# Kernel optimization log

Measured on AMD Instinct MI355X. Metric: run time of the kernel, lower is better.

Reference implementation:

```python
import jax, jax.numpy as jnp
import numpy as np

N_NODES = 1000000
N_EDGES = 2000000
N_FEAT = 11          # QM9 num_features
HIDDEN = 64
N_CLASSES = 19       # QM9 num_classes
BATCH = 128


def setup_inputs() -> dict:
    key = jax.random.key(0)
    k = jax.random.split(key, 8)
    x = jax.random.normal(k[0], (N_NODES, N_FEAT), dtype=jnp.float32)
    edge_index = jax.random.randint(k[1], (2, N_EDGES), 0, N_NODES, dtype=jnp.int64)
    y = jax.random.normal(k[2], (BATCH, N_CLASSES), dtype=jnp.float32)
    batch = jnp.sort(jax.random.randint(k[3], (N_NODES,), 0, BATCH, dtype=jnp.int64))
    # GCNConv params: weight [in, hidden], bias [hidden]
    W_conv = jax.random.normal(k[4], (N_FEAT, HIDDEN), dtype=jnp.float32) / np.sqrt(N_FEAT)
    b_conv = jnp.zeros((HIDDEN,), dtype=jnp.float32)
    # Final linear: [hidden, classes]
    W_lin = jax.random.normal(k[5], (HIDDEN, N_CLASSES), dtype=jnp.float32) / np.sqrt(HIDDEN)
    b_lin = jnp.zeros((N_CLASSES,), dtype=jnp.float32)
    return {"x": x, "edge_index": edge_index, "y": y, "batch": batch,
            "W_conv": W_conv, "b_conv": b_conv, "W_lin": W_lin, "b_lin": b_lin}


def reference(x, edge_index, y, batch, W_conv, b_conv, W_lin, b_lin):
    row, col = edge_index[0], edge_index[1]  # source -> target
    # GCN symmetric normalization (add_self_loops=False): deg over targets
    ones = jnp.ones((edge_index.shape[1],), dtype=x.dtype)
    deg = jax.ops.segment_sum(ones, col, num_segments=N_NODES)
    dinv = jnp.where(deg > 0, jax.lax.rsqrt(jnp.maximum(deg, 1.0)), 0.0)
    norm = dinv[row] * dinv[col]  # [E]
    # Transform then aggregate: gather at source, scatter-add at target
    xw = x @ W_conv                                    # [N, H]
    msgs = xw[row] * norm[:, None]                     # [E, H]
    agg = jax.ops.segment_sum(msgs, col, num_segments=N_NODES) + b_conv
    h = jax.nn.relu(agg)                               # [N, H]
    # global_mean_pool over batch ids (size=BATCH)
    summed = jax.ops.segment_sum(h, batch, num_segments=BATCH)   # [B, H]
    counts = jax.ops.segment_sum(jnp.ones((N_NODES,), dtype=x.dtype), batch, num_segments=BATCH)
    pooled = summed / jnp.maximum(counts, 1.0)[:, None]
    # dropout p=0.5 is identity in eval mode
    return pooled @ W_lin + b_lin                      # [B, classes]
```

## Files before the change

kernel.cpp:

```cpp
#include <hip/hip_runtime.h>

#define N_NODES   1000000
#define N_EDGES   2000000
#define N_FEAT    11
#define HIDDEN    64
#define BATCH     128
#define N_CLASSES 19

#define NPB     2048
#define NBUCK   489
#define BCAP    5120
#define EPB     8192
#define PBLK    245
#define NSLOT   8
#define NCHUNK  3907
#define FROW    24
#define ZOFF    (256 * FROW)

typedef __attribute__((ext_vector_type(8))) short v8s;
typedef __attribute__((ext_vector_type(4))) float v4f;

__device__ __forceinline__ unsigned f2b(float v) {
    unsigned u = __float_as_uint(v);
    return (u + 0x7FFFu + ((u >> 16) & 1u)) >> 16;
}

__global__ __launch_bounds__(1024) void part_kernel(const int* __restrict__ row,
                                                    const int* __restrict__ col,
                                                    int* __restrict__ bcnt,
                                                    int* __restrict__ part) {
    __shared__ int lh[512];
    const int t = threadIdx.x;
    if (t < 512) lh[t] = 0;
    __syncthreads();
    const int q0 = (blockIdx.x * EPB) >> 2;
    const int4* col4 = (const int4*)col;
    const int4* row4 = (const int4*)row;
    const int qa = q0 + t, qb = q0 + 1024 + t;
    const bool va = qa < N_EDGES / 4, vb = qb < N_EDGES / 4;
    int4 ca, ra, cb, rb;
    if (va) { ca = col4[qa]; ra = row4[qa]; }
    if (vb) { cb = col4[qb]; rb = row4[qb]; }
    if (va) {
        atomicAdd(&lh[ca.x >> 11], 1); atomicAdd(&lh[ca.y >> 11], 1);
        atomicAdd(&lh[ca.z >> 11], 1); atomicAdd(&lh[ca.w >> 11], 1);
    }
    if (vb) {
        atomicAdd(&lh[cb.x >> 11], 1); atomicAdd(&lh[cb.y >> 11], 1);
        atomicAdd(&lh[cb.z >> 11], 1); atomicAdd(&lh[cb.w >> 11], 1);
    }
    __syncthreads();
    if (t < NBUCK) {
        int v = lh[t];
        if (v) lh[t] = t * BCAP + atomicAdd(&bcnt[t], v);
    }
    __syncthreads();
    int p;
    if (va) {
        p = atomicAdd(&lh[ca.x >> 11], 1); part[p] = (ra.x << 11) | (ca.x & (NPB - 1));
        p = atomicAdd(&lh[ca.y >> 11], 1); part[p] = (ra.y << 11) | (ca.y & (NPB - 1));
        p = atomicAdd(&lh[ca.z >> 11], 1); part[p] = (ra.z << 11) | (ca.z & (NPB - 1));
        p = atomicAdd(&lh[ca.w >> 11], 1); part[p] = (ra.w << 11) | (ca.w & (NPB - 1));
    }
    if (vb) {
        p = atomicAdd(&lh[cb.x >> 11], 1); part[p] = (rb.x << 11) | (cb.x & (NPB - 1));
        p = atomicAdd(&lh[cb.y >> 11], 1); part[p] = (rb.y << 11) | (cb.y & (NPB - 1));
        p = atomicAdd(&lh[cb.z >> 11], 1); part[p] = (rb.z << 11) | (cb.z & (NPB - 1));
        p = atomicAdd(&lh[cb.w >> 11], 1); part[p] = (rb.w << 11) | (cb.w & (NPB - 1));
    }
}

__global__ __launch_bounds__(512) void sort2_kernel(const int* __restrict__ part,
                                                    const int* __restrict__ bcnt,
                                                    const float* __restrict__ x,
                                                    int* __restrict__ srcs,
                                                    int* __restrict__ nstart,
                                                    unsigned short* __restrict__ ndeg,
                                                    float* __restrict__ dinv,
                                                    unsigned short* __restrict__ xs) {
    __shared__ int cnt[NPB];
    __shared__ int off[NPB];
    __shared__ int tsum[512];
    __shared__ int stage[BCAP];
    const int t = threadIdx.x, b = blockIdx.x;
    for (int i = t; i < NPB; i += 512) cnt[i] = 0;
    __syncthreads();
    const int s0 = b * BCAP, e0 = s0 + bcnt[b];
    for (int j = s0 + t; j < e0; j += 512)
        atomicAdd(&cnt[part[j] & (NPB - 1)], 1);
    __syncthreads();
    const int i0 = t * 4;
    int c[4], s = 0;
#pragma unroll
    for (int q = 0; q < 4; ++q) { c[q] = cnt[i0 + q]; s += c[q]; }
    tsum[t] = s;
    __syncthreads();
    for (int o = 1; o < 512; o <<= 1) {
        int a = (t >= o) ? tsum[t - o] : 0;
        __syncthreads();
        tsum[t] += a;
        __syncthreads();
    }
    int run = tsum[t] - s;
#pragma unroll
    for (int q = 0; q < 4; ++q) { off[i0 + q] = run; run += c[q]; }
    __syncthreads();
    for (int i = t; i < NPB; i += 512) {
        int n = b * NPB + i;
        if (n < N_NODES) {
            int d = cnt[i];
            float dv = d ? rsqrtf((float)d) : 0.0f;
            dinv[n]   = dv;
            ndeg[n]   = (unsigned short)d;
            nstart[n] = s0 + off[i];
            const float* xr = x + (size_t)n * N_FEAT;
            unsigned h[11];
#pragma unroll
            for (int k = 0; k < 11; ++k) h[k] = f2b(dv * xr[k]);
            uint4 A, B;
            A.x = h[0] | (h[1] << 16); A.y = h[2] | (h[3] << 16);
            A.z = h[4] | (h[5] << 16); A.w = h[6] | (h[7] << 16);
            B.x = h[8] | (h[9] << 16); B.y = h[10]; B.z = 0u; B.w = 0u;
            uint4* o = (uint4*)(xs + (size_t)n * 16);
            o[0] = A; o[1] = B;
        }
    }
    __syncthreads();
    for (int j = s0 + t; j < e0; j += 512) {
        int p  = part[j];
        int cl = p & (NPB - 1);
        int pos = atomicAdd(&off[cl], 1);
        stage[pos] = p >> 11;
    }
    __syncthreads();
    const int m = e0 - s0;
    const int m4 = m >> 2;
    int4* d4 = (int4*)(srcs + s0);
    const int4* s4 = (const int4*)stage;
    for (int j = t; j < m4; j += 512) d4[j] = s4[j];
    for (int j = (m4 << 2) + t; j < m; j += 512) srcs[s0 + j] = stage[j];
}

__global__ __launch_bounds__(256) void gather_pool_kernel(
    const int* __restrict__ srcs, const unsigned short* __restrict__ xs,
    const int* __restrict__ nstart, const unsigned short* __restrict__ ndeg,
    const float* __restrict__ dinv, const int* __restrict__ batch,
    const float* __restrict__ Wc, const float* __restrict__ bc,
    float* __restrict__ pooled, float* __restrict__ countsf) {
    __shared__ unsigned short fb16[ZOFF + 8];
    __shared__ int   sj0[256];
    __shared__ int   sdeg[256];
    __shared__ float sdinv[256];
    __shared__ int   sbid[256];
    __shared__ int   sperm[256];
    __shared__ int   dcnt[32];
    __shared__ int   doff[32];
    __shared__ float pbuf[2 * HIDDEN];
    __shared__ int   pcnt[NSLOT];
    const int t = threadIdx.x, lane = t & 63, w = t >> 6;
    const int quad = lane >> 4;
    const int base = blockIdx.x * 256;
    {
        int n = base + t;
        bool v = n < N_NODES;
        sj0[t]   = v ? nstart[n] : 0;
        sdeg[t]  = v ? (int)ndeg[n] : 0;
        sdinv[t] = v ? dinv[n] : 0.0f;
        sbid[t]  = v ? batch[n] : -1;
    }
    if (t < 2 * HIDDEN) pbuf[t] = 0.0f;
    if (t < NSLOT) pcnt[t] = 0;
    if (t < 32)    dcnt[t] = 0;
    if (t < 4)     ((unsigned*)(fb16 + ZOFF))[t] = 0u;
    __syncthreads();
    const int bid0 = sbid[0];
    {
        int bid = sbid[t];
        if (bid >= 0) {
            int slot = bid - bid0;
            if (slot >= 0 && slot < NSLOT) atomicAdd(&pcnt[slot], 1);
            else atomicAdd(&countsf[bid], 1.0f);
        }
    }
    int mybin = sdeg[t] < 31 ? sdeg[t] : 31;
    atomicAdd(&dcnt[mybin], 1);
    __syncthreads();
    if (t < 32) {
        int r = 0;
        for (int i = 0; i < t; ++i) r += dcnt[i];
        doff[t] = r;
    }
    __syncthreads();
    int pos = atomicAdd(&doff[mybin], 1);
    sperm[pos] = t;
    __syncthreads();

    {
        int i  = sperm[t];
        int j0 = sj0[i], d = sdeg[i];
        float acc[11];
#pragma unroll
        for (int k = 0; k < 11; ++k) acc[k] = 0.0f;
        for (int j = j0; j < j0 + d; ++j) {
            int r = srcs[j];
            const uint4* xr = (const uint4*)(xs + (size_t)r * 16);
            uint4 A = xr[0];
            uint2 B = *(const uint2*)(xr + 1);
            acc[0]  += __uint_as_float(A.x << 16);
            acc[1]  += __uint_as_float(A.x & 0xFFFF0000u);
            acc[2]  += __uint_as_float(A.y << 16);
            acc[3]  += __uint_as_float(A.y & 0xFFFF0000u);
            acc[4]  += __uint_as_float(A.z << 16);
            acc[5]  += __uint_as_float(A.z & 0xFFFF0000u);
            acc[6]  += __uint_as_float(A.w << 16);
            acc[7]  += __uint_as_float(A.w & 0xFFFF0000u);
            acc[8]  += __uint_as_float(B.x << 16);
            acc[9]  += __uint_as_float(B.x & 0xFFFF0000u);
            acc[10] += __uint_as_float(B.y << 16);
        }
        unsigned hb[11];
#pragma unroll
        for (int k = 0; k < 11; ++k) hb[k] = f2b(acc[k]);
        uint4 U0, U1;
        U0.x = hb[0] | (hb[1] << 16); U0.y = hb[2]  | (hb[3] << 16);
        U0.z = hb[4] | (hb[5] << 16); U0.w = hb[6]  | (hb[7] << 16);
        U1.x = hb[8] | (hb[9] << 16); U1.y = hb[10]; U1.z = 0u; U1.w = 0u;
        uint4* wp = (uint4*)(fb16 + i * FROW);
        wp[0] = U0; wp[1] = U1;
    }
    __syncthreads();

    const int nch = w * 16 + (lane & 15);
    union { v8s v; unsigned short us[8]; } bf;
#pragma unroll
    for (int j = 0; j < 8; ++j) {
        int k = quad * 8 + j;
        bf.us[j] = (k < 11) ? (unsigned short)f2b(Wc[k * HIDDEN + nch]) : (unsigned short)0;
    }
    const float bias_lane = bc[nch];
    float acc0 = 0.0f, acc1 = 0.0f;
#pragma unroll 4
    for (int mtile = 0; mtile < 16; ++mtile) {
        const v8s* ap = (quad < 2)
            ? (const v8s*)(fb16 + (mtile * 16 + (lane & 15)) * FROW + quad * 8)
            : (const v8s*)(fb16 + ZOFF);
        v8s a = *ap;
        v4f d = __builtin_amdgcn_mfma_f32_16x16x32_bf16(a, bf.v, (v4f){0.f, 0.f, 0.f, 0.f}, 0, 0, 0);
#pragma unroll
        for (int r = 0; r < 4; ++r) {
            int node = mtile * 16 + quad * 4 + r;
            int bid  = sbid[node];
            if (bid >= 0) {
                float h = fmaxf(fmaf(sdinv[node], d[r], bias_lane), 0.0f);
                int slot = bid - bid0;
                if (slot == 0)      acc0 += h;
                else if (slot == 1) acc1 += h;
                else atomicAdd(&pooled[(size_t)bid * HIDDEN + nch], h);
            }
        }
    }
    atomicAdd(&pbuf[nch], acc0);
    atomicAdd(&pbuf[HIDDEN + nch], acc1);
    __syncthreads();
    for (int s = w; s < 2; s += 4) {
        int c = pcnt[s];
        if (c > 0) {
            atomicAdd(&pooled[(size_t)(bid0 + s) * HIDDEN + lane], pbuf[s * HIDDEN + lane]);
            if (lane == 0) atomicAdd(&countsf[bid0 + s], (float)c);
        }
    }
}

__global__ void final_kernel(const float* __restrict__ pooled, const float* __restrict__ counts,
                             const float* __restrict__ Wl, const float* __restrict__ bl,
                             float* __restrict__ out) {
    int i = blockIdx.x * blockDim.x + threadIdx.x;
    if (i >= BATCH * N_CLASSES) return;
    int b = i / N_CLASSES;
    int c = i - b * N_CLASSES;
    float inv = 1.0f / fmaxf(counts[b], 1.0f);
    float s = bl[c];
#pragma unroll 8
    for (int h = 0; h < HIDDEN; ++h)
        s = fmaf(pooled[b * HIDDEN + h] * inv, Wl[h * N_CLASSES + c], s);
    out[i] = s;
}

extern "C" void kernel_launch(void* const* d_in, const int* in_sizes, int n_in,
                              void* d_out, int out_size, void* d_ws, size_t ws_size,
                              hipStream_t stream) {
    const float* x     = (const float*)d_in[0];
    const int*   ei    = (const int*)d_in[1];
    const int*   batch = (const int*)d_in[3];
    const float* Wc    = (const float*)d_in[4];
    const float* bc    = (const float*)d_in[5];
    const float* Wl    = (const float*)d_in[6];
    const float* bl    = (const float*)d_in[7];
    float*       out   = (float*)d_out;

    int*            bcnt    = (int*)d_ws;
    float*          pooled  = (float*)(bcnt + 512);
    float*          countsf = pooled + BATCH * HIDDEN;
    unsigned short* xs      = (unsigned short*)(countsf + BATCH);
    int*            nstart  = (int*)(xs + (size_t)N_NODES * 16);
    unsigned short* ndeg    = (unsigned short*)(nstart + N_NODES);
    float*          dinv    = (float*)(ndeg + N_NODES);
    int*            part    = (int*)(dinv + N_NODES);
    int*            srcs    = part + (size_t)NBUCK * BCAP;

    size_t zero_bytes = (512 + BATCH * HIDDEN + BATCH) * 4;
    hipMemsetAsync(d_ws, 0, zero_bytes, stream);

    const int* row = ei;
    const int* col = ei + N_EDGES;

    part_kernel <<<PBLK, 1024, 0, stream>>>(row, col, bcnt, part);
    sort2_kernel<<<NBUCK, 512, 0, stream>>>(part, bcnt, x, srcs, nstart, ndeg, dinv, xs);
    gather_pool_kernel<<<NCHUNK, 256, 0, stream>>>(srcs, xs, nstart, ndeg, dinv,
                                                   batch, Wc, bc, pooled, countsf);
    final_kernel<<<(BATCH * N_CLASSES + 255) / 256, 256, 0, stream>>>(pooled, countsf, Wl, bl, out);
}
```

Measured before the change: 221.4 us.

## Stage bucket edges in LDS, widen sort block, batch gather loads by eight

Result: slower. 230.3 us (+4.0%).

```diff
diff --git a/kernel.cpp b/kernel.cpp
--- a/kernel.cpp
+++ b/kernel.cpp
@@ -70,42 +70,44 @@
     }
 }
 
-__global__ __launch_bounds__(512) void sort2_kernel(const int* __restrict__ part,
-                                                    const int* __restrict__ bcnt,
-                                                    const float* __restrict__ x,
-                                                    int* __restrict__ srcs,
-                                                    int* __restrict__ nstart,
-                                                    unsigned short* __restrict__ ndeg,
-                                                    float* __restrict__ dinv,
-                                                    unsigned short* __restrict__ xs) {
+__global__ __launch_bounds__(1024) void sort2_kernel(const int* __restrict__ part,
+                                                     const int* __restrict__ bcnt,
+                                                     const float* __restrict__ x,
+                                                     int* __restrict__ srcs,
+                                                     int* __restrict__ nstart,
+                                                     unsigned short* __restrict__ ndeg,
+                                                     float* __restrict__ dinv,
+                                                     unsigned short* __restrict__ xs) {
     __shared__ int cnt[NPB];
     __shared__ int off[NPB];
-    __shared__ int tsum[512];
+    __shared__ int tsum[1024];
     __shared__ int stage[BCAP];
+    __shared__ int outb[BCAP];
     const int t = threadIdx.x, b = blockIdx.x;
-    for (int i = t; i < NPB; i += 512) cnt[i] = 0;
-    __syncthreads();
-    const int s0 = b * BCAP, e0 = s0 + bcnt[b];
-    for (int j = s0 + t; j < e0; j += 512)
-        atomicAdd(&cnt[part[j] & (NPB - 1)], 1);
-    __syncthreads();
-    const int i0 = t * 4;
-    int c[4], s = 0;
-#pragma unroll
-    for (int q = 0; q < 4; ++q) { c[q] = cnt[i0 + q]; s += c[q]; }
+    for (int i = t; i < NPB; i += 1024) cnt[i] = 0;
+    __syncthreads();
+    const int s0 = b * BCAP, m = bcnt[b];
+    for (int j = t; j < m; j += 1024) {
+        int v = part[s0 + j];
+        stage[j] = v;
+        atomicAdd(&cnt[v & (NPB - 1)], 1);
+    }
+    __syncthreads();
+    const int i0 = t * 2;
+    int c0 = cnt[i0], c1 = cnt[i0 + 1];
+    int s = c0 + c1;
     tsum[t] = s;
     __syncthreads();
-    for (int o = 1; o < 512; o <<= 1) {
+    for (int o = 1; o < 1024; o <<= 1) {
         int a = (t >= o) ? tsum[t - o] : 0;
         __syncthreads();
         tsum[t] += a;
         __syncthreads();
     }
     int run = tsum[t] - s;
-#pragma unroll
-    for (int q = 0; q < 4; ++q) { off[i0 + q] = run; run += c[q]; }
-    __syncthreads();
-    for (int i = t; i < NPB; i += 512) {
+    off[i0] = run; off[i0 + 1] = run + c0;
+    __syncthreads();
+    for (int i = t; i < NPB; i += 1024) {
         int n = b * NPB + i;
         if (n < N_NODES) {
             int d = cnt[i];
@@ -126,19 +128,18 @@
         }
     }
     __syncthreads();
-    for (int j = s0 + t; j < e0; j += 512) {
-        int p  = part[j];
+    for (int j = t; j < m; j += 1024) {
+        int p  = stage[j];
         int cl = p & (NPB - 1);
         int pos = atomicAdd(&off[cl], 1);
-        stage[pos] = p >> 11;
-    }
-    __syncthreads();
-    const int m = e0 - s0;
+        outb[pos] = p >> 11;
+    }
+    __syncthreads();
     const int m4 = m >> 2;
     int4* d4 = (int4*)(srcs + s0);
-    const int4* s4 = (const int4*)stage;
-    for (int j = t; j < m4; j += 512) d4[j] = s4[j];
-    for (int j = (m4 << 2) + t; j < m; j += 512) srcs[s0 + j] = stage[j];
+    const int4* s4 = (const int4*)outb;
+    for (int j = t; j < m4; j += 1024) d4[j] = s4[j];
+    for (int j = (m4 << 2) + t; j < m; j += 1024) srcs[s0 + j] = outb[j];
 }
 
 __global__ __launch_bounds__(256) void gather_pool_kernel(
@@ -198,25 +199,35 @@
     {
         int i  = sperm[t];
         int j0 = sj0[i], d = sdeg[i];
+        const int e = j0 + d;
         float acc[11];
 #pragma unroll
         for (int k = 0; k < 11; ++k) acc[k] = 0.0f;
-        for (int j = j0; j < j0 + d; ++j) {
-            int r = srcs[j];
-            const uint4* xr = (const uint4*)(xs + (size_t)r * 16);
-            uint4 A = xr[0];
-            uint2 B = *(const uint2*)(xr + 1);
-            acc[0]  += __uint_as_float(A.x << 16);
-            acc[1]  += __uint_as_float(A.x & 0xFFFF0000u);
-            acc[2]  += __uint_as_float(A.y << 16);
-            acc[3]  += __uint_as_float(A.y & 0xFFFF0000u);
-            acc[4]  += __uint_as_float(A.z << 16);
-            acc[5]  += __uint_as_float(A.z & 0xFFFF0000u);
-            acc[6]  += __uint_as_float(A.w << 16);
-            acc[7]  += __uint_as_float(A.w & 0xFFFF0000u);
-            acc[8]  += __uint_as_float(B.x << 16);
-            acc[9]  += __uint_as_float(B.x & 0xFFFF0000u);
-            acc[10] += __uint_as_float(B.y << 16);
+        for (int j = j0; j < e; j += 8) {
+            uint4 A[8]; uint2 B[8]; float mq[8];
+#pragma unroll
+            for (int q = 0; q < 8; ++q) {
+                int jq = (j + q < e) ? j + q : j;
+                mq[q] = (q == 0 || j + q < e) ? 1.0f : 0.0f;
+                int r = srcs[jq];
+                const uint4* p = (const uint4*)(xs + (size_t)r * 16);
+                A[q] = p[0];
+                B[q] = *(const uint2*)(p + 1);
+            }
+#pragma unroll
+            for (int q = 0; q < 8; ++q) {
+                acc[0]  = fmaf(mq[q], __uint_as_float(A[q].x << 16),         acc[0]);
+                acc[1]  = fmaf(mq[q], __uint_as_float(A[q].x & 0xFFFF0000u), acc[1]);
+                acc[2]  = fmaf(mq[q], __uint_as_float(A[q].y << 16),         acc[2]);
+                acc[3]  = fmaf(mq[q], __uint_as_float(A[q].y & 0xFFFF0000u), acc[3]);
+                acc[4]  = fmaf(mq[q], __uint_as_float(A[q].z << 16),         acc[4]);
+                acc[5]  = fmaf(mq[q], __uint_as_float(A[q].z & 0xFFFF0000u), acc[5]);
+                acc[6]  = fmaf(mq[q], __uint_as_float(A[q].w << 16),         acc[6]);
+                acc[7]  = fmaf(mq[q], __uint_as_float(A[q].w & 0xFFFF0000u), acc[7]);
+                acc[8]  = fmaf(mq[q], __uint_as_float(B[q].x << 16),         acc[8]);
+                acc[9]  = fmaf(mq[q], __uint_as_float(B[q].x & 0xFFFF0000u), acc[9]);
+                acc[10] = fmaf(mq[q], __uint_as_float(B[q].y << 16),         acc[10]);
+            }
         }
         unsigned hb[11];
 #pragma unroll
@@ -315,7 +326,7 @@
     const int* col = ei + N_EDGES;
 
     part_kernel <<<PBLK, 1024, 0, stream>>>(row, col, bcnt, part);
-    sort2_kernel<<<NBUCK, 512, 0, stream>>>(part, bcnt, x, srcs, nstart, ndeg, dinv, xs);
+    sort2_kernel<<<NBUCK, 1024, 0, stream>>>(part, bcnt, x, srcs, nstart, ndeg, dinv, xs);
     gather_pool_kernel<<<NCHUNK, 256, 0, stream>>>(srcs, xs, nstart, ndeg, dinv,
                                                    batch, Wc, bc, pooled, countsf);
     final_kernel<<<(BATCH * N_CLASSES + 255) / 256, 256, 0, stream>>>(pooled, countsf, Wl, bl, out);
```
